# Kernel tuning notes

Measured on AMD Instinct MI355X. Metric: run time of the kernel, lower is better.

## Reference

```python
import jax, jax.numpy as jnp
import numpy as np

ALPHA = 0.2  # LeakyReLU negative slope
NEG_BIG = -9e15

def setup_inputs() -> dict:
    key = jax.random.key(0)
    k1, k2, k3, k4 = jax.random.split(key, 4)
    N, F_IN, F_OUT = 8192, 128, 128
    h = jax.random.normal(k1, (N, F_IN), dtype=jnp.float32)
    adj = jax.random.randint(k2, (N, N), 0, 2, dtype=jnp.int32)
    # xavier-uniform-ish params
    W = jax.random.normal(k3, (F_IN, F_OUT), dtype=jnp.float32) * (1.0 / np.sqrt(F_IN))
    a = jax.random.normal(k4, (2 * F_OUT, 1), dtype=jnp.float32) * (1.0 / np.sqrt(2 * F_OUT))
    return {"h": h, "adj": adj, "W": W, "a": a}

def reference(h, adj, W, a):
    # Wh: [N, F_OUT]
    Wh = h @ W
    F_out = Wh.shape[1]
    # a_input @ a == (Wh @ a1)_i + (Wh @ a2)_j  (same math, no N^2*2F tensor)
    a1 = a[:F_out, 0]   # [F_OUT]
    a2 = a[F_out:, 0]   # [F_OUT]
    e = (Wh @ a1)[:, None] + (Wh @ a2)[None, :]        # [N, N]
    e = jnp.where(e >= 0, e, ALPHA * e)                # LeakyReLU(0.2)
    scores = jnp.where(adj > 0, e, NEG_BIG)
    attention = jax.nn.softmax(scores, axis=1)         # row-wise
    # dropout skipped (eval mode / training=False)
    return attention @ Wh                              # [N, F_OUT]
```

## Files before the change

kernel.cpp:

```cpp
#include <hip/hip_runtime.h>
#include <hip/hip_bf16.h>

#define N 8192
#define FD 128

typedef __attribute__((ext_vector_type(4))) float f4;
typedef __attribute__((ext_vector_type(4))) int i32x4;
typedef __attribute__((ext_vector_type(4))) unsigned int u32x4;
typedef __attribute__((ext_vector_type(4))) unsigned short us4;
typedef __attribute__((ext_vector_type(8))) __bf16 bf16x8;

__device__ __forceinline__ unsigned short bfbits(float x){
  __bf16 b = (__bf16)x;
  return __builtin_bit_cast(unsigned short, b);
}

__global__ __launch_bounds__(256) void k1_wh(const float* __restrict__ h,
                                             const float* __restrict__ W,
                                             float* __restrict__ Wh,
                                             unsigned short* __restrict__ WhbT){
  __shared__ float Wl[64*128];
  __shared__ float hT[128*33];
  int t = threadIdx.x;
  int i0 = blockIdx.x * 32;
  {
    int r  = t >> 3;
    int k0 = (t & 7) * 16;
    const f4* src = (const f4*)&h[(size_t)(i0 + r)*FD + k0];
    #pragma unroll
    for (int q = 0; q < 4; ++q){
      f4 v = src[q];
      #pragma unroll
      for (int e = 0; e < 4; ++e) hT[(k0 + q*4 + e)*33 + r] = v[e];
    }
  }
  int f0 = (t & 31) * 4;
  int r0 = (t >> 5) * 4;
  float acc[4][4] = {};
  for (int half = 0; half < 2; ++half){
    __syncthreads();
    #pragma unroll
    for (int v = 0; v < 8; ++v){
      int idx = (v*256 + t)*4;
      *(f4*)&Wl[idx] = *(const f4*)&W[half*8192 + idx];
    }
    __syncthreads();
    for (int k2 = 0; k2 < 64; ++k2){
      f4 wv = *(const f4*)&Wl[k2*FD + f0];
      f4 hv = *(const f4*)&hT[(half*64 + k2)*33 + r0];
      #pragma unroll
      for (int ri = 0; ri < 4; ++ri)
        #pragma unroll
        for (int fi = 0; fi < 4; ++fi)
          acc[ri][fi] = __builtin_fmaf(hv[ri], wv[fi], acc[ri][fi]);
    }
  }
  #pragma unroll
  for (int ri = 0; ri < 4; ++ri){
    f4 o = {acc[ri][0], acc[ri][1], acc[ri][2], acc[ri][3]};
    *(f4*)&Wh[(size_t)(i0 + r0 + ri)*FD + f0] = o;
  }
  #pragma unroll
  for (int fi = 0; fi < 4; ++fi){
    us4 o;
    #pragma unroll
    for (int ri = 0; ri < 4; ++ri) o[ri] = bfbits(acc[ri][fi]);
    *(us4*)&WhbT[(size_t)(f0 + fi)*N + i0 + r0] = o;
  }
}

__global__ __launch_bounds__(256) void k2_s(const float* __restrict__ Wh,
                                            const float* __restrict__ a,
                                            float* __restrict__ s1,
                                            float* __restrict__ s2){
  int i = blockIdx.x*256 + threadIdx.x;
  const f4* row = (const f4*)&Wh[(size_t)i*FD];
  const f4* a1 = (const f4*)a;
  const f4* a2 = (const f4*)&a[FD];
  float x1 = 0.f, x2 = 0.f;
  #pragma unroll
  for (int q = 0; q < 32; ++q){
    f4 w = row[q], va = a1[q], vb = a2[q];
    #pragma unroll
    for (int e = 0; e < 4; ++e){
      x1 = __builtin_fmaf(w[e], va[e], x1);
      x2 = __builtin_fmaf(w[e], vb[e], x2);
    }
  }
  s1[i] = x1; s2[i] = x2;
}

__global__ __launch_bounds__(256) void k3_max(const float* __restrict__ s2,
                                              float* __restrict__ M2){
  __shared__ float red[4];
  int t = threadIdx.x;
  float m = -3.0e38f;
  for (int i = t; i < N; i += 256) m = fmaxf(m, s2[i]);
  #pragma unroll
  for (int d = 1; d < 64; d <<= 1) m = fmaxf(m, __shfl_xor(m, d, 64));
  if ((t & 63) == 0) red[t >> 6] = m;
  __syncthreads();
  if (t == 0) *M2 = fmaxf(fmaxf(red[0], red[1]), fmaxf(red[2], red[3]));
}

__global__ __launch_bounds__(256,2) void k4_flash(const int* __restrict__ adj,
    const unsigned short* __restrict__ WhbT,
    const float* __restrict__ s1, const float* __restrict__ s2,
    const float* __restrict__ M2p,
    float* __restrict__ partial, float* __restrict__ denomp, int njc){
  int t = threadIdx.x;
  int wv = t >> 6, lane = t & 63;
  int lrow = lane & 15, lgrp = lane >> 4;
  int i0 = blockIdx.x * 128 + wv * 32;
  int jlen = N / njc;
  int jstart = blockIdx.y * jlen;
  float M2 = *M2p;
  float s1a = s1[i0 + lrow], s1b = s1[i0 + 16 + lrow];
  float ea = s1a + M2, eb = s1b + M2;
  float ma = fmaxf(ea, 0.2f*ea), mb = fmaxf(eb, 0.2f*eb);

  f4 acc[2][8];
  #pragma unroll
  for (int x = 0; x < 2; ++x)
    #pragma unroll
    for (int n = 0; n < 8; ++n) acc[x][n] = (f4){0.f,0.f,0.f,0.f};
  float da = 0.f, db = 0.f;

  const i32x4* adj4 = (const i32x4*)adj;
  size_t rowa = ((size_t)(i0 + lrow) * N) >> 2;
  size_t rowb = rowa + (size_t)(16*N)/4;

  for (int js = 0; js < jlen/32; ++js){
    int jb = jstart + js*32 + lgrp*8;
    i32x4 A0 = adj4[rowa + (jb>>2)];
    i32x4 A1 = adj4[rowa + (jb>>2) + 1];
    i32x4 B0 = adj4[rowb + (jb>>2)];
    i32x4 B1 = adj4[rowb + (jb>>2) + 1];
    f4 s2a = *(const f4*)&s2[jb];
    f4 s2b = *(const f4*)&s2[jb+4];
    u32x4 braw[8];
    #pragma unroll
    for (int n = 0; n < 8; ++n)
      braw[n] = *(const u32x4*)&WhbT[(size_t)(n*16 + lrow)*N + jb];

    bf16x8 fa, fb;
    #pragma unroll
    for (int e = 0; e < 8; ++e){
      float sj = (e < 4) ? s2a[e & 3] : s2b[e & 3];
      int av = (e < 4) ? A0[e & 3] : A1[e & 3];
      int bv = (e < 4) ? B0[e & 3] : B1[e & 3];
      float t0 = s1a + sj;
      float p0 = av ? __expf(fmaxf(t0, 0.2f*t0) - ma) : 0.f;
      float t1 = s1b + sj;
      float p1 = bv ? __expf(fmaxf(t1, 0.2f*t1) - mb) : 0.f;
      da += p0; db += p1;
      fa[e] = (__bf16)p0; fb[e] = (__bf16)p1;
    }
    #pragma unroll
    for (int n = 0; n < 8; ++n){
      bf16x8 bb = __builtin_bit_cast(bf16x8, braw[n]);
      acc[0][n] = __builtin_amdgcn_mfma_f32_16x16x32_bf16(fa, bb, acc[0][n], 0, 0, 0);
      acc[1][n] = __builtin_amdgcn_mfma_f32_16x16x32_bf16(fb, bb, acc[1][n], 0, 0, 0);
    }
  }

  da += __shfl_xor(da, 16, 64); da += __shfl_xor(da, 32, 64);
  db += __shfl_xor(db, 16, 64); db += __shfl_xor(db, 32, 64);
  if (lgrp == 0){
    denomp[(size_t)blockIdx.y*N + i0 + lrow] = da;
    denomp[(size_t)blockIdx.y*N + i0 + 16 + lrow] = db;
  }
  float* pb = partial + (size_t)blockIdx.y * N * FD;
  #pragma unroll
  for (int x = 0; x < 2; ++x)
    #pragma unroll
    for (int n = 0; n < 8; ++n)
      #pragma unroll
      for (int r = 0; r < 4; ++r)
        pb[(size_t)(i0 + x*16 + lgrp*4 + r)*FD + n*16 + lrow] = acc[x][n][r];
}

__global__ __launch_bounds__(256) void k5_fin(const float* __restrict__ partial,
    const float* __restrict__ denomp, float* __restrict__ out, int njc){
  int g = blockIdx.x*256 + threadIdx.x;
  int i = g >> 7;
  float num = 0.f, den = 0.f;
  for (int c = 0; c < njc; ++c) num += partial[(size_t)c*N*FD + g];
  for (int c = 0; c < njc; ++c) den += denomp[(size_t)c*N + i];
  out[g] = num / den;
}

extern "C" void kernel_launch(void* const* d_in, const int* in_sizes, int n_in,
                              void* d_out, int out_size, void* d_ws, size_t ws_size,
                              hipStream_t stream){
  const float* h   = (const float*)d_in[0];
  const int*   adj = (const int*)d_in[1];
  const float* W   = (const float*)d_in[2];
  const float* a   = (const float*)d_in[3];
  float* out = (float*)d_out;
  char* ws = (char*)d_ws;

  unsigned short* WhbT = (unsigned short*)ws;
  float* Wh = (float*)(ws + (size_t)(2u<<20));
  float* s1 = (float*)(ws + (size_t)(6u<<20));
  float* s2 = (float*)(ws + (size_t)(6u<<20) + 32768);
  float* M2 = (float*)(ws + (size_t)(6u<<20) + 65536);
  float* denomp  = (float*)(ws + (size_t)(7u<<20));
  float* partial = (float*)(ws + (size_t)(8u<<20));

  size_t chunk = (size_t)N * FD * sizeof(float);
  int njc = 1;
  if (ws_size > ((size_t)(8u<<20))){
    size_t m = (ws_size - (size_t)(8u<<20)) / chunk;
    njc = (m >= 16) ? 16 : (m >= 8) ? 8 : (m >= 4) ? 4 : (m >= 2) ? 2 : 1;
  }

  hipLaunchKernelGGL(k1_wh,  dim3(256),      dim3(256), 0, stream, h, W, Wh, WhbT);
  hipLaunchKernelGGL(k2_s,   dim3(32),       dim3(256), 0, stream, Wh, a, s1, s2);
  hipLaunchKernelGGL(k3_max, dim3(1),        dim3(256), 0, stream, s2, M2);
  hipLaunchKernelGGL(k4_flash, dim3(64, njc), dim3(256), 0, stream,
                     adj, WhbT, s1, s2, M2, partial, denomp, njc);
  hipLaunchKernelGGL(k5_fin, dim3(N*FD/256), dim3(256), 0, stream, partial, denomp, out, njc);
}
```

Baseline: 485.3 us.

## Pre-swizzle Wh into MFMA fragment layout, single-tile waves, prefetch adj, exp2 scores

k1 now writes bf16 Wh directly in the per-lane MFMA B-fragment order, so each lane in k4 loads its fragment with one contiguous 16-byte read instead of strided rows of a transposed matrix. Each wave now handles 16 rows instead of 32, the grid doubles to 128 blocks, and launch bounds allow 4 blocks per CU. Adjacency and s2 values for the next step are loaded one iteration ahead. Scores are prescaled by log2(e) so exp2 replaces exp, the row sums are computed with an extra MFMA against a ones vector, and the column-split count is capped at 8. The trade-off is that each B-fragment load is now reused by one MFMA instead of two, and the denominator sums bf16-rounded probabilities.

```diff
diff --git a/kernel.cpp b/kernel.cpp
--- a/kernel.cpp
+++ b/kernel.cpp
@@ -3,11 +3,11 @@
 
 #define N 8192
 #define FD 128
+#define LOG2E 1.4426950408889634f
 
 typedef __attribute__((ext_vector_type(4))) float f4;
 typedef __attribute__((ext_vector_type(4))) int i32x4;
 typedef __attribute__((ext_vector_type(4))) unsigned int u32x4;
-typedef __attribute__((ext_vector_type(4))) unsigned short us4;
 typedef __attribute__((ext_vector_type(8))) __bf16 bf16x8;
 
 __device__ __forceinline__ unsigned short bfbits(float x){
@@ -18,7 +18,7 @@
 __global__ __launch_bounds__(256) void k1_wh(const float* __restrict__ h,
                                              const float* __restrict__ W,
                                              float* __restrict__ Wh,
-                                             unsigned short* __restrict__ WhbT){
+                                             unsigned short* __restrict__ Bsw){
   __shared__ float Wl[64*128];
   __shared__ float hT[128*33];
   int t = threadIdx.x;
@@ -60,19 +60,23 @@
     f4 o = {acc[ri][0], acc[ri][1], acc[ri][2], acc[ri][3]};
     *(f4*)&Wh[(size_t)(i0 + r0 + ri)*FD + f0] = o;
   }
-  #pragma unroll
-  for (int fi = 0; fi < 4; ++fi){
-    us4 o;
-    #pragma unroll
-    for (int ri = 0; ri < 4; ++ri) o[ri] = bfbits(acc[ri][fi]);
-    *(us4*)&WhbT[(size_t)(f0 + fi)*N + i0 + r0] = o;
+  int jblk = blockIdx.x;
+  int n  = f0 >> 4;
+  int fl = f0 & 15;
+  #pragma unroll
+  for (int ri = 0; ri < 4; ++ri){
+    int k = r0 + ri;
+    size_t base = (((size_t)jblk*8 + n)*64 + ((k>>3)<<4))*8 + (k&7);
+    #pragma unroll
+    for (int fi = 0; fi < 4; ++fi)
+      Bsw[base + (size_t)(fl + fi)*8] = bfbits(acc[ri][fi]);
   }
 }
 
 __global__ __launch_bounds__(256) void k2_s(const float* __restrict__ Wh,
                                             const float* __restrict__ a,
-                                            float* __restrict__ s1,
-                                            float* __restrict__ s2){
+                                            float* __restrict__ s1L,
+                                            float* __restrict__ s2L){
   int i = blockIdx.x*256 + threadIdx.x;
   const f4* row = (const f4*)&Wh[(size_t)i*FD];
   const f4* a1 = (const f4*)a;
@@ -87,97 +91,100 @@
       x2 = __builtin_fmaf(w[e], vb[e], x2);
     }
   }
-  s1[i] = x1; s2[i] = x2;
-}
-
-__global__ __launch_bounds__(256) void k3_max(const float* __restrict__ s2,
-                                              float* __restrict__ M2){
+  s1L[i] = x1 * LOG2E; s2L[i] = x2 * LOG2E;
+}
+
+__global__ __launch_bounds__(256) void k3_max(const float* __restrict__ s2L,
+                                              float* __restrict__ M2L){
   __shared__ float red[4];
   int t = threadIdx.x;
   float m = -3.0e38f;
-  for (int i = t; i < N; i += 256) m = fmaxf(m, s2[i]);
+  for (int i = t; i < N; i += 256) m = fmaxf(m, s2L[i]);
   #pragma unroll
   for (int d = 1; d < 64; d <<= 1) m = fmaxf(m, __shfl_xor(m, d, 64));
   if ((t & 63) == 0) red[t >> 6] = m;
   __syncthreads();
-  if (t == 0) *M2 = fmaxf(fmaxf(red[0], red[1]), fmaxf(red[2], red[3]));
-}
-
-__global__ __launch_bounds__(256,2) void k4_flash(const int* __restrict__ adj,
-    const unsigned short* __restrict__ WhbT,
-    const float* __restrict__ s1, const float* __restrict__ s2,
+  if (t == 0) *M2L = fmaxf(fmaxf(red[0], red[1]), fmaxf(red[2], red[3]));
+}
+
+__global__ __launch_bounds__(256,4) void k4_flash(const int* __restrict__ adj,
+    const unsigned short* __restrict__ Bsw,
+    const float* __restrict__ s1L, const float* __restrict__ s2L,
     const float* __restrict__ M2p,
     float* __restrict__ partial, float* __restrict__ denomp, int njc){
   int t = threadIdx.x;
   int wv = t >> 6, lane = t & 63;
   int lrow = lane & 15, lgrp = lane >> 4;
-  int i0 = blockIdx.x * 128 + wv * 32;
+  int i0w = blockIdx.x * 64 + wv * 16;
+  int row = i0w + lrow;
   int jlen = N / njc;
   int jstart = blockIdx.y * jlen;
+  int iters = jlen / 32;
   float M2 = *M2p;
-  float s1a = s1[i0 + lrow], s1b = s1[i0 + 16 + lrow];
-  float ea = s1a + M2, eb = s1b + M2;
-  float ma = fmaxf(ea, 0.2f*ea), mb = fmaxf(eb, 0.2f*eb);
-
-  f4 acc[2][8];
-  #pragma unroll
-  for (int x = 0; x < 2; ++x)
-    #pragma unroll
-    for (int n = 0; n < 8; ++n) acc[x][n] = (f4){0.f,0.f,0.f,0.f};
-  float da = 0.f, db = 0.f;
+  float s1a = s1L[row];
+  float ea = s1a + M2;
+  float maL = fmaxf(ea, 0.2f*ea);
+
+  f4 acc[8];
+  #pragma unroll
+  for (int n = 0; n < 8; ++n) acc[n] = (f4){0.f,0.f,0.f,0.f};
+  f4 accd = (f4){0.f,0.f,0.f,0.f};
+
+  u32x4 onesbits = (u32x4){0x3F803F80u,0x3F803F80u,0x3F803F80u,0x3F803F80u};
+  bf16x8 ones = __builtin_bit_cast(bf16x8, onesbits);
 
   const i32x4* adj4 = (const i32x4*)adj;
-  size_t rowa = ((size_t)(i0 + lrow) * N) >> 2;
-  size_t rowb = rowa + (size_t)(16*N)/4;
-
-  for (int js = 0; js < jlen/32; ++js){
-    int jb = jstart + js*32 + lgrp*8;
-    i32x4 A0 = adj4[rowa + (jb>>2)];
-    i32x4 A1 = adj4[rowa + (jb>>2) + 1];
-    i32x4 B0 = adj4[rowb + (jb>>2)];
-    i32x4 B1 = adj4[rowb + (jb>>2) + 1];
-    f4 s2a = *(const f4*)&s2[jb];
-    f4 s2b = *(const f4*)&s2[jb+4];
+  const f4* s2v = (const f4*)s2L;
+  size_t rbase = ((size_t)row * N) >> 2;
+
+  int jb = jstart + lgrp*8;
+  i32x4 c0 = adj4[rbase + (jb>>2)];
+  i32x4 c1 = adj4[rbase + (jb>>2) + 1];
+  f4 za = s2v[jb>>2], zb = s2v[(jb>>2)+1];
+
+  for (int js = 0; js < iters; ++js){
+    i32x4 u0 = c0, u1 = c1; f4 ya = za, yb = zb;
+    int jn = jb + 32;
+    if (jn >= jstart + jlen) jn = jstart + lgrp*8;
+    c0 = adj4[rbase + (jn>>2)];
+    c1 = adj4[rbase + (jn>>2) + 1];
+    za = s2v[jn>>2]; zb = s2v[(jn>>2)+1];
+
+    int jtile = jb >> 5;
     u32x4 braw[8];
     #pragma unroll
     for (int n = 0; n < 8; ++n)
-      braw[n] = *(const u32x4*)&WhbT[(size_t)(n*16 + lrow)*N + jb];
-
-    bf16x8 fa, fb;
+      braw[n] = *(const u32x4*)&Bsw[((((size_t)jtile*8 + n)*64) + lane)*8];
+
+    bf16x8 fa;
     #pragma unroll
     for (int e = 0; e < 8; ++e){
-      float sj = (e < 4) ? s2a[e & 3] : s2b[e & 3];
-      int av = (e < 4) ? A0[e & 3] : A1[e & 3];
-      int bv = (e < 4) ? B0[e & 3] : B1[e & 3];
-      float t0 = s1a + sj;
-      float p0 = av ? __expf(fmaxf(t0, 0.2f*t0) - ma) : 0.f;
-      float t1 = s1b + sj;
-      float p1 = bv ? __expf(fmaxf(t1, 0.2f*t1) - mb) : 0.f;
-      da += p0; db += p1;
-      fa[e] = (__bf16)p0; fb[e] = (__bf16)p1;
-    }
-    #pragma unroll
-    for (int n = 0; n < 8; ++n){
-      bf16x8 bb = __builtin_bit_cast(bf16x8, braw[n]);
-      acc[0][n] = __builtin_amdgcn_mfma_f32_16x16x32_bf16(fa, bb, acc[0][n], 0, 0, 0);
-      acc[1][n] = __builtin_amdgcn_mfma_f32_16x16x32_bf16(fb, bb, acc[1][n], 0, 0, 0);
-    }
-  }
-
-  da += __shfl_xor(da, 16, 64); da += __shfl_xor(da, 32, 64);
-  db += __shfl_xor(db, 16, 64); db += __shfl_xor(db, 32, 64);
-  if (lgrp == 0){
-    denomp[(size_t)blockIdx.y*N + i0 + lrow] = da;
-    denomp[(size_t)blockIdx.y*N + i0 + 16 + lrow] = db;
+      float sj = (e < 4) ? ya[e] : yb[e-4];
+      int av   = (e < 4) ? u0[e] : u1[e-4];
+      float x  = s1a + sj;
+      float lr = fmaxf(x, 0.2f*x);
+      float p  = av ? __builtin_amdgcn_exp2f(lr - maL) : 0.f;
+      fa[e] = (__bf16)p;
+    }
+    accd = __builtin_amdgcn_mfma_f32_16x16x32_bf16(fa, ones, accd, 0, 0, 0);
+    #pragma unroll
+    for (int n = 0; n < 8; ++n)
+      acc[n] = __builtin_amdgcn_mfma_f32_16x16x32_bf16(fa,
+                 __builtin_bit_cast(bf16x8, braw[n]), acc[n], 0, 0, 0);
+    jb += 32;
+  }
+
+  if (lrow == 0){
+    #pragma unroll
+    for (int r = 0; r < 4; ++r)
+      denomp[(size_t)blockIdx.y*N + i0w + lgrp*4 + r] = accd[r];
   }
   float* pb = partial + (size_t)blockIdx.y * N * FD;
   #pragma unroll
-  for (int x = 0; x < 2; ++x)
-    #pragma unroll
-    for (int n = 0; n < 8; ++n)
-      #pragma unroll
-      for (int r = 0; r < 4; ++r)
-        pb[(size_t)(i0 + x*16 + lgrp*4 + r)*FD + n*16 + lrow] = acc[x][n][r];
+  for (int n = 0; n < 8; ++n)
+    #pragma unroll
+    for (int r = 0; r < 4; ++r)
+      pb[(size_t)(i0w + lgrp*4 + r)*FD + n*16 + lrow] = acc[n][r];
 }
 
 __global__ __launch_bounds__(256) void k5_fin(const float* __restrict__ partial,
@@ -200,11 +207,11 @@
   float* out = (float*)d_out;
   char* ws = (char*)d_ws;
 
-  unsigned short* WhbT = (unsigned short*)ws;
-  float* Wh = (float*)(ws + (size_t)(2u<<20));
-  float* s1 = (float*)(ws + (size_t)(6u<<20));
-  float* s2 = (float*)(ws + (size_t)(6u<<20) + 32768);
-  float* M2 = (float*)(ws + (size_t)(6u<<20) + 65536);
+  unsigned short* Bsw = (unsigned short*)ws;
+  float* Wh  = (float*)(ws + (size_t)(2u<<20));
+  float* s1L = (float*)(ws + (size_t)(6u<<20));
+  float* s2L = (float*)(ws + (size_t)(6u<<20) + 32768);
+  float* M2L = (float*)(ws + (size_t)(6u<<20) + 65536);
   float* denomp  = (float*)(ws + (size_t)(7u<<20));
   float* partial = (float*)(ws + (size_t)(8u<<20));
 
@@ -212,13 +219,13 @@
   int njc = 1;
   if (ws_size > ((size_t)(8u<<20))){
     size_t m = (ws_size - (size_t)(8u<<20)) / chunk;
-    njc = (m >= 16) ? 16 : (m >= 8) ? 8 : (m >= 4) ? 4 : (m >= 2) ? 2 : 1;
-  }
-
-  hipLaunchKernelGGL(k1_wh,  dim3(256),      dim3(256), 0, stream, h, W, Wh, WhbT);
-  hipLaunchKernelGGL(k2_s,   dim3(32),       dim3(256), 0, stream, Wh, a, s1, s2);
-  hipLaunchKernelGGL(k3_max, dim3(1),        dim3(256), 0, stream, s2, M2);
-  hipLaunchKernelGGL(k4_flash, dim3(64, njc), dim3(256), 0, stream,
-                     adj, WhbT, s1, s2, M2, partial, denomp, njc);
+    njc = (m >= 8) ? 8 : (m >= 4) ? 4 : (m >= 2) ? 2 : 1;
+  }
+
+  hipLaunchKernelGGL(k1_wh,  dim3(256), dim3(256), 0, stream, h, W, Wh, Bsw);
+  hipLaunchKernelGGL(k2_s,   dim3(32),  dim3(256), 0, stream, Wh, a, s1L, s2L);
+  hipLaunchKernelGGL(k3_max, dim3(1),   dim3(256), 0, stream, s2L, M2L);
+  hipLaunchKernelGGL(k4_flash, dim3(128, njc), dim3(256), 0, stream,
+                     adj, Bsw, s1L, s2L, M2L, partial, denomp, njc);
   hipLaunchKernelGGL(k5_fin, dim3(N*FD/256), dim3(256), 0, stream, partial, denomp, out, njc);
 }
```

Result: no change. 489.5 us (+0.9%).
